# Kernel optimization log

Hardware: AMD Instinct MI355X
Metric: run time of the kernel (lower is better)

## Reference

```python
import jax, jax.numpy as jnp
import numpy as np

GROUP = 4      # number of groups in the batch dim
SHARED_GP = 4  # conv groups for q/k 1x1 convs
C = 512
N = 4096
B = 4          # B_all = GROUP * B = 16
EPS_LN = 1e-6
EPS_Z = 1e-6


def _phi(x):
    return jax.nn.relu(x) + 1.0


def _grouped_1x1(x, W):
    # x: [B, C, N], W: [g, C/g, C/g] block-diagonal 1x1 conv weights
    Bx, Cx, Nx = x.shape
    g = W.shape[0]
    xg = x.reshape(Bx, g, Cx // g, Nx)
    return jnp.einsum('goc,bgcn->bgon', W, xg).reshape(Bx, Cx, Nx)


def _ln(x, w, b, eps=EPS_LN):
    m = jnp.mean(x, axis=-1, keepdims=True)
    v = jnp.mean(jnp.square(x - m), axis=-1, keepdims=True)
    return (x - m) * jax.lax.rsqrt(v + eps) * w + b


def setup_inputs() -> dict:
    key = jax.random.key(0)
    ks = jax.random.split(key, 12)
    cg = C // SHARED_GP
    s = 1.0 / np.sqrt(C)
    return {
        'x': jax.random.normal(ks[0], (GROUP * B, C, N), dtype=jnp.float32),
        'Wq': jax.random.normal(ks[1], (SHARED_GP, cg, cg), dtype=jnp.float32) / np.sqrt(cg),
        'Wk': jax.random.normal(ks[2], (SHARED_GP, cg, cg), dtype=jnp.float32) / np.sqrt(cg),
        'Wv': jax.random.normal(ks[3], (C, C), dtype=jnp.float32) * s,
        'Wphi': jax.random.normal(ks[4], (C, C), dtype=jnp.float32) * s,
        'ln1_w': jnp.ones((C,), dtype=jnp.float32),
        'ln1_b': jnp.zeros((C,), dtype=jnp.float32),
        'fc1_w': jax.random.normal(ks[5], (4 * C, C), dtype=jnp.float32) * s,
        'fc1_b': jnp.zeros((4 * C,), dtype=jnp.float32),
        'fc2_w': jax.random.normal(ks[6], (C, 4 * C), dtype=jnp.float32) / np.sqrt(4 * C),
        'fc2_b': jnp.zeros((C,), dtype=jnp.float32),
        'ln2_w': jnp.ones((C,), dtype=jnp.float32),
        'ln2_b': jnp.zeros((C,), dtype=jnp.float32),
    }


def reference(x, Wq, Wk, Wv, Wphi, ln1_w, ln1_b, fc1_w, fc1_b, fc2_w, fc2_b, ln2_w, ln2_b):
    B_all, Cc, Nn = x.shape
    g = GROUP
    Bb = B_all // g
    first, rest = x[:Bb], x[Bb:]             # [B,C,N], [M,C,N] with M=(g-1)*B
    M = (g - 1) * Bb

    q = _phi(_grouped_1x1(rest, Wq))          # [M,C,N]
    k0 = _phi(_grouped_1x1(first, Wk))        # [B,C,N]
    v0 = jnp.einsum('oc,bcn->bon', Wv, first)  # [B,C,N]
    phi_first = jnp.einsum('oc,bcn->bon', Wphi, first)
    phi_rest = jnp.einsum('oc,bcn->bon', Wphi, rest)

    # expand first-group k/v across the (g-1) query groups
    k = jnp.broadcast_to(k0[None], (g - 1, Bb, Cc, Nn)).reshape(M, Cc, Nn)
    v = jnp.broadcast_to(v0[None], (g - 1, Bb, Cc, Nn)).reshape(M, Cc, Nn)

    Qg = jnp.broadcast_to(k0.mean(axis=2, keepdims=True)[None],
                          (g - 1, Bb, Cc, 1)).reshape(M, Cc, 1)
    alpha = jax.nn.softmax(jnp.sum(Qg * k, axis=1, keepdims=True), axis=-1) * Nn  # [M,1,N]
    k_hat = k * alpha

    # linear attention: kv = k_hat @ v^T / sqrt(C)
    kv = jnp.einsum('mcn,mdn->mcd', k_hat, v) / jnp.sqrt(jnp.asarray(Cc, x.dtype))  # [M,C,C]
    k_sum = jnp.sum(k_hat, axis=-1)                                  # [M,C]
    z = 1.0 / (jnp.einsum('mcn,mc->mn', q, k_sum)[:, None, :] + EPS_Z)  # [M,1,N]
    y = jnp.einsum('mcn,mcd->mdn', q, kv) * z * phi_rest              # [M,C,N]

    y_first = jnp.mean(y, axis=0, keepdims=True) * phi_first          # [B,C,N]
    out_first = _ln((first + y_first).transpose(0, 2, 1), ln1_w, ln1_b)  # [B,N,C]
    h = jax.nn.relu(out_first @ fc1_w.T + fc1_b)
    out_first = out_first + h @ fc2_w.T + fc2_b
    out_first = jax.nn.relu(_ln(out_first, ln2_w, ln2_b))
    out_first = out_first.transpose(0, 2, 1)                          # [B,C,N]
    return jnp.concatenate([out_first, rest], axis=0)
```

## Files before the change

kernel.cpp:

```cpp
#include <hip/hip_runtime.h>

#define N_DIM 4096
#define C_DIM 512
#define CN_ ((long)C_DIM * (long)N_DIM)

typedef unsigned short ushort_t;
typedef __attribute__((ext_vector_type(8))) short bf16x8;
typedef __attribute__((ext_vector_type(4))) float f32x4;

typedef const __attribute__((address_space(1))) unsigned int* gas_t;
typedef __attribute__((address_space(3))) unsigned int* las_t;
#define GLOAD(g, l) __builtin_amdgcn_global_load_lds((gas_t)(g), (las_t)(l), 16, 0, 0)

__device__ __forceinline__ ushort_t f2b(float f) {
    unsigned u = __builtin_bit_cast(unsigned, f);
    u += 0x7fffu + ((u >> 16) & 1u);
    return (ushort_t)(u >> 16);
}
__device__ __forceinline__ float b2f(ushort_t s) {
    return __builtin_bit_cast(float, (unsigned)s << 16);
}

enum { EPI_NONE = 0, EPI_PHI = 1, EPI_RELU_BIAS = 2, EPI_RES_BIAS = 3, EPI_PRE = 4 };

#define STAGE(q, koff) { \
    GLOAD(ap0 + (koff), &Als[q][la0]); \
    GLOAD(ap1 + (koff), &Als[q][la1]); \
    GLOAD(bp0 + (koff), &Bls[q][la0]); \
    GLOAD(bp1 + (koff), &Bls[q][la1]); }

#define COMPUTE(q) { \
    bf16x8 af[4], bfv[4]; \
    _Pragma("unroll") for (int m_ = 0; m_ < 4; ++m_) \
        af[m_] = *(const bf16x8*)&Als[q][(wr + m_ * 16 + fr) * 32 + rsw]; \
    _Pragma("unroll") for (int nf_ = 0; nf_ < 4; ++nf_) \
        bfv[nf_] = *(const bf16x8*)&Bls[q][(wc + nf_ * 16 + fr) * 32 + rsw]; \
    _Pragma("unroll") for (int m_ = 0; m_ < 4; ++m_) \
        _Pragma("unroll") for (int nf_ = 0; nf_ < 4; ++nf_) \
            acc[m_][nf_] = __builtin_amdgcn_mfma_f32_16x16x32_bf16( \
                af[m_], bfv[nf_], acc[m_][nf_], 0, 0, 0); }

#define KLOOP(K_) { \
    STAGE(0, 0); \
    __syncthreads(); \
    int kk_ = 0; \
    while (true) { \
        if (kk_ + 32 < (K_)) STAGE(1, kk_ + 32); \
        COMPUTE(0); \
        __syncthreads(); \
        kk_ += 32; \
        if (kk_ >= (K_)) break; \
        if (kk_ + 32 < (K_)) STAGE(0, kk_ + 32); \
        COMPUTE(1); \
        __syncthreads(); \
        kk_ += 32; \
        if (kk_ >= (K_)) break; \
    } }

template<int EPI, bool GROUPED, bool OBF, bool DEN, bool QGS>
__global__ __launch_bounds__(256, 3) void mfma_gemm(
    const ushort_t* __restrict__ Wb, const ushort_t* __restrict__ A,
    void* __restrict__ OUTV, const float* __restrict__ bias,
    const ushort_t* __restrict__ auxb, const float* __restrict__ auxf,
    int K, int O, int a_rstride, long a_zstride, long o_zstride, long auxb_zstride,
    int xt, int yt)
{
    __shared__ ushort_t Als[2][128 * 32];
    __shared__ ushort_t Bls[2][128 * 32];
    const int tid = threadIdx.x;

    const int L = blockIdx.x;
    const int gpx = (gridDim.x >> 3) / xt;
    const int xcd = L & 7;
    const int j = L >> 3;
    const int xtile = j % xt;
    const int g = xcd * gpx + j / xt;
    const int ytile = g % yt;
    const int z = g / yt;

    const int o0 = xtile * 128;
    const int n0 = ytile * 128;
    const ushort_t* Az = A + (long)z * a_zstride;
    const ushort_t* Wp = Wb;
    int kbase = 0, obase = o0;
    if (GROUPED) { int gg = o0 >> 7; Wp = Wb + (long)gg * (128 * 128); kbase = gg << 7; obase = 0; }

    const int w = tid >> 6, l = tid & 63;
    const int lr = l >> 2, lg = l & 3;
    const int rA0 = w * 32 + lr, rA1 = w * 32 + 16 + lr;
    const int gA0 = lg ^ ((rA0 >> 1) & 3), gA1 = lg ^ ((rA1 >> 1) & 3);
    const ushort_t* ap0 = Az + (long)(n0 + rA0) * a_rstride + kbase + gA0 * 8;
    const ushort_t* ap1 = Az + (long)(n0 + rA1) * a_rstride + kbase + gA1 * 8;
    const ushort_t* bp0 = Wp + (long)(obase + rA0) * K + gA0 * 8;
    const ushort_t* bp1 = Wp + (long)(obase + rA1) * K + gA1 * 8;
    const int la0 = (w * 32) * 32, la1 = (w * 32 + 16) * 32;

    const int wr = (w >> 1) * 64, wc = (w & 1) * 64;
    const int fr = l & 15, ks = l >> 4;
    const int rsw = (ks ^ ((fr >> 1) & 3)) << 3;

    f32x4 acc[4][4];
#pragma unroll
    for (int m = 0; m < 4; ++m)
#pragma unroll
        for (int nf = 0; nf < 4; ++nf) acc[m][nf] = f32x4{0.f, 0.f, 0.f, 0.f};

    KLOOP(K);

    float dsum[4][4];
    if (DEN) {
#pragma unroll
        for (int m = 0; m < 4; ++m)
#pragma unroll
            for (int j2 = 0; j2 < 4; ++j2) dsum[m][j2] = 0.f;
    }
    float qsum[4];
    if (QGS) {
#pragma unroll
        for (int nf = 0; nf < 4; ++nf) qsum[nf] = 0.f;
    }

#pragma unroll
    for (int m = 0; m < 4; ++m) {
#pragma unroll
        for (int nf = 0; nf < 4; ++nf) {
            const int oo = o0 + wc + nf * 16 + fr;
            float bval = 0.f;
            if (EPI == EPI_RELU_BIAS || EPI == EPI_RES_BIAS) bval = bias[oo];
            float kw = 0.f;
            if (DEN) kw = bias[((z & 3) << 9) + oo];
#pragma unroll
            for (int j2 = 0; j2 < 4; ++j2) {
                const int nn = n0 + wr + m * 16 + ks * 4 + j2;
                const long ridx = (long)nn * O + oo;
                float v = acc[m][nf][j2];
                if (EPI == EPI_PHI)            v = fmaxf(v, 0.f) + 1.f;
                else if (EPI == EPI_RELU_BIAS) v = fmaxf(v + bval, 0.f);
                else if (EPI == EPI_RES_BIAS)  v = v + bval + b2f(auxb[(long)z * auxb_zstride + ridx]);
                else if (EPI == EPI_PRE)       v = b2f(auxb[(long)z * auxb_zstride + ridx]) + auxf[ridx] * v;
                if (DEN) dsum[m][j2] += v * kw;
                if (QGS) qsum[nf] += v;
                if (OBF) ((ushort_t*)OUTV)[(long)z * o_zstride + ridx] = f2b(v);
                else     ((float*)OUTV)[(long)z * o_zstride + ridx] = v;
            }
        }
    }

    if (DEN) {
#pragma unroll
        for (int m = 0; m < 4; ++m)
#pragma unroll
            for (int j2 = 0; j2 < 4; ++j2) {
                float d = dsum[m][j2];
                d += __shfl_xor(d, 1); d += __shfl_xor(d, 2);
                d += __shfl_xor(d, 4); d += __shfl_xor(d, 8);
                if (fr == 0) {
                    const int nn = n0 + wr + m * 16 + ks * 4 + j2;
                    atomicAdd((float*)&auxf[(long)z * N_DIM + nn], d);
                }
            }
    }
    if (QGS) {
#pragma unroll
        for (int nf = 0; nf < 4; ++nf) {
            float d = qsum[nf];
            d += __shfl_xor(d, 16);
            d += __shfl_xor(d, 32);
            if (ks == 0) {
                const int oo = o0 + wc + nf * 16 + fr;
                atomicAdd((float*)&auxf[((long)z << 9) + oo], d);
            }
        }
    }
}

__global__ __launch_bounds__(256, 3) void kv_mfma(
    const ushort_t* __restrict__ v0c, const ushort_t* __restrict__ khat,
    float* __restrict__ kvp)
{
    __shared__ ushort_t Als[2][128 * 32];
    __shared__ ushort_t Bls[2][128 * 32];
    const int tid = threadIdx.x;
    const int L = blockIdx.x;
    const int gpx = (gridDim.x >> 3) >> 2;
    const int xcd = L & 7;
    const int j = L >> 3;
    const int xtile = j & 3;
    const int g = xcd * gpx + (j >> 2);
    const int ytile = g & 3;
    const int z = g >> 2;
    const int c0 = xtile * 128, d0 = ytile * 128;
    const int b = z >> 3, nch = z & 7;

    const int w = tid >> 6, l = tid & 63;
    const int lr = l >> 2, lg = l & 3;
    const int rA0 = w * 32 + lr, rA1 = w * 32 + 16 + lr;
    const int gA0 = lg ^ ((rA0 >> 1) & 3), gA1 = lg ^ ((rA1 >> 1) & 3);
    const ushort_t* Ab = v0c + (long)b * CN_ + nch * 512;
    const ushort_t* Bb = khat + (long)b * CN_ + nch * 512;
    const ushort_t* ap0 = Ab + (long)(d0 + rA0) * N_DIM + gA0 * 8;
    const ushort_t* ap1 = Ab + (long)(d0 + rA1) * N_DIM + gA1 * 8;
    const ushort_t* bp0 = Bb + (long)(c0 + rA0) * N_DIM + gA0 * 8;
    const ushort_t* bp1 = Bb + (long)(c0 + rA1) * N_DIM + gA1 * 8;
    const int la0 = (w * 32) * 32, la1 = (w * 32 + 16) * 32;

    const int wr = (w >> 1) * 64, wc = (w & 1) * 64;
    const int fr = l & 15, ks = l >> 4;
    const int rsw = (ks ^ ((fr >> 1) & 3)) << 3;

    f32x4 acc[4][4];
#pragma unroll
    for (int m = 0; m < 4; ++m)
#pragma unroll
        for (int nf = 0; nf < 4; ++nf) acc[m][nf] = f32x4{0.f, 0.f, 0.f, 0.f};

    KLOOP(512);

    float* KV = kvp + ((long)(nch * 4 + b)) * 262144;
#pragma unroll
    for (int m = 0; m < 4; ++m)
#pragma unroll
        for (int nf = 0; nf < 4; ++nf) {
            const int cc = c0 + wc + nf * 16 + fr;
#pragma unroll
            for (int j2 = 0; j2 < 4; ++j2) {
                const int dd = d0 + wr + m * 16 + ks * 4 + j2;
                KV[(long)dd * 512 + cc] = acc[m][nf][j2];
            }
        }
}

__global__ __launch_bounds__(256) void cvt_scale8(
    const float* __restrict__ kvp, ushort_t* __restrict__ out)
{
    const float s = 0.044194173824159216f;
    const long i = ((long)blockIdx.x * 256 + threadIdx.x) * 4;
    const int b = (int)(i >> 18);
    const long j = i & 262143;
    float4 a = make_float4(0.f, 0.f, 0.f, 0.f);
#pragma unroll
    for (int nch = 0; nch < 8; ++nch) {
        float4 v = *(const float4*)&kvp[((long)(nch * 4 + b)) * 262144 + j];
        a.x += v.x; a.y += v.y; a.z += v.z; a.w += v.w;
    }
    union { ushort_t sh[4]; uint2 u; } p;
    p.sh[0] = f2b(a.x * s); p.sh[1] = f2b(a.y * s);
    p.sh[2] = f2b(a.z * s); p.sh[3] = f2b(a.w * s);
    *(uint2*)&out[i] = p.u;
}

__global__ __launch_bounds__(256, 2) void ybar_gemm(
    const ushort_t* __restrict__ q12, const ushort_t* __restrict__ kvT,
    const ushort_t* __restrict__ xT12, const ushort_t* __restrict__ Wphi_b,
    const float* __restrict__ den12, ushort_t* __restrict__ y12)
{
    __shared__ ushort_t Als[2][128 * 32];
    __shared__ ushort_t Bls[2][128 * 32];
    __shared__ ushort_t Cls[2][128 * 32];
    __shared__ ushort_t Dls[2][128 * 32];
    const int tid = threadIdx.x;
    const int L = blockIdx.x;
    const int gpx = (gridDim.x >> 3) >> 2;
    const int xcd = L & 7;
    const int j = L >> 3;
    const int xtile = j & 3;
    const int g = xcd * gpx + (j >> 2);
    const int ytile = g & 31;
    const int mm = g >> 5;
    const int o0 = xtile * 128, n0 = ytile * 128;

    const int w = tid >> 6, l = tid & 63;
    const int lr = l >> 2, lg = l & 3;
    const int rA0 = w * 32 + lr, rA1 = w * 32 + 16 + lr;
    const int gA0 = lg ^ ((rA0 >> 1) & 3), gA1 = lg ^ ((rA1 >> 1) & 3);
    const long aoff0 = (long)(n0 + rA0) * 512 + gA0 * 8;
    const long aoff1 = (long)(n0 + rA1) * 512 + gA1 * 8;
    const long boff0 = (long)(o0 + rA0) * 512 + gA0 * 8;
    const long boff1 = (long)(o0 + rA1) * 512 + gA1 * 8;
    const int la0 = (w * 32) * 32, la1 = (w * 32 + 16) * 32;

    const int wr = (w >> 1) * 64, wc = (w & 1) * 64;
    const int fr = l & 15, ks = l >> 4;
    const int rsw = (ks ^ ((fr >> 1) & 3)) << 3;

    const ushort_t* pa0 = xT12 + (long)mm * CN_ + aoff0;
    const ushort_t* pa1 = xT12 + (long)mm * CN_ + aoff1;
    const ushort_t* pb0 = Wphi_b + boff0;
    const ushort_t* pb1 = Wphi_b + boff1;
    const ushort_t* qa0 = q12 + (long)mm * CN_ + aoff0;
    const ushort_t* qa1 = q12 + (long)mm * CN_ + aoff1;
    const ushort_t* kb0 = kvT + (long)(mm & 3) * 262144 + boff0;
    const ushort_t* kb1 = kvT + (long)(mm & 3) * 262144 + boff1;

    f32x4 accP[4][4], accQ[4][4];
#pragma unroll
    for (int m = 0; m < 4; ++m)
#pragma unroll
        for (int nf = 0; nf < 4; ++nf) {
            accP[m][nf] = f32x4{0.f, 0.f, 0.f, 0.f};
            accQ[m][nf] = f32x4{0.f, 0.f, 0.f, 0.f};
        }

#define STAGE2(q, koff) { \
    GLOAD(pa0 + (koff), &Als[q][la0]); GLOAD(pa1 + (koff), &Als[q][la1]); \
    GLOAD(pb0 + (koff), &Bls[q][la0]); GLOAD(pb1 + (koff), &Bls[q][la1]); \
    GLOAD(qa0 + (koff), &Cls[q][la0]); GLOAD(qa1 + (koff), &Cls[q][la1]); \
    GLOAD(kb0 + (koff), &Dls[q][la0]); GLOAD(kb1 + (koff), &Dls[q][la1]); }

#define COMPUTE2(q) { \
    bf16x8 af[4], bfv[4], cf[4], df[4]; \
    _Pragma("unroll") for (int m_ = 0; m_ < 4; ++m_) { \
        af[m_] = *(const bf16x8*)&Als[q][(wr + m_ * 16 + fr) * 32 + rsw]; \
        cf[m_] = *(const bf16x8*)&Cls[q][(wr + m_ * 16 + fr) * 32 + rsw]; } \
    _Pragma("unroll") for (int nf_ = 0; nf_ < 4; ++nf_) { \
        bfv[nf_] = *(const bf16x8*)&Bls[q][(wc + nf_ * 16 + fr) * 32 + rsw]; \
        df[nf_] = *(const bf16x8*)&Dls[q][(wc + nf_ * 16 + fr) * 32 + rsw]; } \
    _Pragma("unroll") for (int m_ = 0; m_ < 4; ++m_) \
        _Pragma("unroll") for (int nf_ = 0; nf_ < 4; ++nf_) { \
            accP[m_][nf_] = __builtin_amdgcn_mfma_f32_16x16x32_bf16( \
                af[m_], bfv[nf_], accP[m_][nf_], 0, 0, 0); \
            accQ[m_][nf_] = __builtin_amdgcn_mfma_f32_16x16x32_bf16( \
                cf[m_], df[nf_], accQ[m_][nf_], 0, 0, 0); } }

    STAGE2(0, 0);
    __syncthreads();
    int kk = 0;
    while (true) {
        if (kk + 32 < 512) STAGE2(1, kk + 32);
        COMPUTE2(0);
        __syncthreads();
        kk += 32;
        if (kk >= 512) break;
        if (kk + 32 < 512) STAGE2(0, kk + 32);
        COMPUTE2(1);
        __syncthreads();
        kk += 32;
        if (kk >= 512) break;
    }
#undef STAGE2
#undef COMPUTE2

    const float* D = den12 + (long)mm * N_DIM;
    ushort_t* Y = y12 + (long)mm * CN_;
#pragma unroll
    for (int m = 0; m < 4; ++m) {
        float zr[4];
#pragma unroll
        for (int j2 = 0; j2 < 4; ++j2)
            zr[j2] = 1.f / (D[n0 + wr + m * 16 + ks * 4 + j2] + 1e-6f);
#pragma unroll
        for (int nf = 0; nf < 4; ++nf) {
            const int oo = o0 + wc + nf * 16 + fr;
#pragma unroll
            for (int j2 = 0; j2 < 4; ++j2) {
                const int nn = n0 + wr + m * 16 + ks * 4 + j2;
                Y[(long)nn * 512 + oo] = f2b(accQ[m][nf][j2] * zr[j2] * accP[m][nf][j2]);
            }
        }
    }
}

__global__ __launch_bounds__(256) void ybar_reduce(
    const ushort_t* __restrict__ y12, float* __restrict__ ybar)
{
    const long i = ((long)blockIdx.x * 256 + threadIdx.x) * 8;
    float s[8] = {0.f, 0.f, 0.f, 0.f, 0.f, 0.f, 0.f, 0.f};
    for (int mm = 0; mm < 12; ++mm) {
        uint4 u = *(const uint4*)&y12[(long)mm * CN_ + i];
        const ushort_t* us = (const ushort_t*)&u;
#pragma unroll
        for (int j = 0; j < 8; ++j) s[j] += b2f(us[j]);
    }
#pragma unroll
    for (int j = 0; j < 8; ++j) s[j] *= (1.f / 12.f);
    *(float4*)&ybar[i] = make_float4(s[0], s[1], s[2], s[3]);
    *(float4*)&ybar[i + 4] = make_float4(s[4], s[5], s[6], s[7]);
}

template<int ALPHA>
__global__ __launch_bounds__(256) void transpose_b2b(
    const ushort_t* __restrict__ in, ushort_t* __restrict__ out,
    const float* __restrict__ alpha, float* __restrict__ ksum)
{
    __shared__ ushort_t t[64][72];
    const int tid = threadIdx.x;
    const int n0 = blockIdx.x * 64, c0 = blockIdx.y * 64, z = blockIdx.z;
    const ushort_t* I = in + (long)z * CN_;
    ushort_t* O = out + (long)z * CN_;
    const int r = tid >> 2, s8 = (tid & 3) * 16;
    uint4 u0 = *(const uint4*)&I[(long)(n0 + r) * 512 + c0 + s8];
    uint4 u1 = *(const uint4*)&I[(long)(n0 + r) * 512 + c0 + s8 + 8];
    *(uint4*)&t[r][s8] = u0;
    *(uint4*)&t[r][s8 + 8] = u1;
    __syncthreads();
    union { ushort_t sh[16]; uint4 u[2]; } p;
#pragma unroll
    for (int i = 0; i < 16; ++i) {
        ushort_t v = t[s8 + i][r];
        if (ALPHA) v = f2b(b2f(v) * alpha[(long)z * N_DIM + n0 + s8 + i]);
        p.sh[i] = v;
    }
    uint4* dst = (uint4*)&O[(long)(c0 + r) * N_DIM + n0 + s8];
    dst[0] = p.u[0]; dst[1] = p.u[1];
    if (ALPHA) {
        const int c = tid & 63, q = tid >> 6;
        float s = 0.f;
#pragma unroll
        for (int i = 0; i < 16; ++i) {
            const int n = q * 16 + i;
            s += b2f(t[n][c]) * alpha[(long)z * N_DIM + n0 + n];
        }
        atomicAdd(&ksum[((long)z << 9) + c0 + c], s);
    }
}

__global__ __launch_bounds__(256) void cvt_all(
    const float* __restrict__ s0, ushort_t* __restrict__ d0,
    const float* __restrict__ s1, ushort_t* __restrict__ d1,
    const float* __restrict__ s2, ushort_t* __restrict__ d2,
    const float* __restrict__ s3, ushort_t* __restrict__ d3,
    const float* __restrict__ s4, ushort_t* __restrict__ d4,
    const float* __restrict__ s5, ushort_t* __restrict__ d5)
{
    long i = ((long)blockIdx.x * 256 + threadIdx.x) * 4;
    const float* s; ushort_t* d; long off;
    if (i < 65536)        { s = s0; d = d0; off = i; }
    else if (i < 131072)  { s = s1; d = d1; off = i - 65536; }
    else if (i < 393216)  { s = s2; d = d2; off = i - 131072; }
    else if (i < 655360)  { s = s3; d = d3; off = i - 393216; }
    else if (i < 1703936) { s = s4; d = d4; off = i - 655360; }
    else                  { s = s5; d = d5; off = i - 1703936; }
    float4 v = *(const float4*)&s[off];
    union { ushort_t sh[4]; uint2 u; } p;
    p.sh[0] = f2b(v.x); p.sh[1] = f2b(v.y); p.sh[2] = f2b(v.z); p.sh[3] = f2b(v.w);
    *(uint2*)&d[off] = p.u;
}

template<int PASSZ>
__global__ __launch_bounds__(256) void transpose_f2b(
    const float* __restrict__ in, ushort_t* __restrict__ out,
    int rows, int cols, long in_z, long out_z, float* __restrict__ passout)
{
    __shared__ float t[64][65];
    const int tid = threadIdx.x;
    const int n0 = blockIdx.x * 64, c0 = blockIdx.y * 64;
    const int z = blockIdx.z;
    const float* I = in + (long)z * in_z;
    ushort_t* Ot = out + (long)z * out_z;
    const int r = tid >> 2, s4 = (tid & 3) * 16;
    float4 raw[4];
#pragma unroll
    for (int i = 0; i < 16; i += 4) {
        float4 v = *(const float4*)&I[(long)(c0 + r) * cols + n0 + s4 + i];
        raw[i >> 2] = v;
        t[r][s4 + i] = v.x; t[r][s4 + i + 1] = v.y;
        t[r][s4 + i + 2] = v.z; t[r][s4 + i + 3] = v.w;
    }
    if (PASSZ && z >= 4) {
        float* P = passout + (long)z * in_z + (long)(c0 + r) * cols + n0 + s4;
#pragma unroll
        for (int i = 0; i < 4; ++i) *(float4*)&P[i * 4] = raw[i];
    }
    __syncthreads();
    union { ushort_t s[16]; uint4 u[2]; } pk;
#pragma unroll
    for (int i = 0; i < 16; ++i) pk.s[i] = f2b(t[s4 + i][r]);
    uint4* dst = (uint4*)&Ot[(long)(n0 + r) * rows + c0 + s4];
    dst[0] = pk.u[0]; dst[1] = pk.u[1];
}

__global__ __launch_bounds__(256) void dot_rows(
    const ushort_t* __restrict__ X, const float* __restrict__ w,
    float* __restrict__ out, float scale)
{
    const int tid = threadIdx.x;
    const int rn = tid >> 2, cs = (tid & 3) * 128;
    const int z = blockIdx.y;
    const int n = blockIdx.x * 64 + rn;
    const ushort_t* row = X + (long)z * CN_ + (long)n * C_DIM;
    const float* wz = w + (long)(z & 3) * C_DIM;
    float s = 0.f;
    for (int i = 0; i < 128; i += 8) {
        uint4 u = *(const uint4*)&row[cs + i];
        const ushort_t* us = (const ushort_t*)&u;
#pragma unroll
        for (int k2 = 0; k2 < 8; ++k2) s += b2f(us[k2]) * wz[cs + i + k2];
    }
    s += __shfl_xor(s, 1); s += __shfl_xor(s, 2);
    if ((tid & 3) == 0) out[(long)z * N_DIM + n] = s * scale;
}

__global__ __launch_bounds__(256) void softmax_alpha(
    const float* __restrict__ logits, float* __restrict__ alpha)
{
    int b = blockIdx.x, tid = threadIdx.x;
    const float* L = logits + (long)b * N_DIM;
    float* A = alpha + (long)b * N_DIM;
    float lv[16];
    float mx = -3.4e38f;
#pragma unroll
    for (int i = 0; i < 4; i++) {
        float4 v = *(const float4*)&L[tid * 4 + i * 1024];
        lv[4 * i + 0] = v.x; lv[4 * i + 1] = v.y; lv[4 * i + 2] = v.z; lv[4 * i + 3] = v.w;
        mx = fmaxf(mx, fmaxf(fmaxf(v.x, v.y), fmaxf(v.z, v.w)));
    }
    __shared__ float red[8];
    float m = mx;
#pragma unroll
    for (int off = 32; off; off >>= 1) m = fmaxf(m, __shfl_down(m, off, 64));
    int wid = tid >> 6, lane = tid & 63;
    if (lane == 0) red[wid] = m;
    __syncthreads();
    m = fmaxf(fmaxf(red[0], red[1]), fmaxf(red[2], red[3]));
    float e[16], s = 0.f;
#pragma unroll
    for (int i = 0; i < 16; i++) { e[i] = expf(lv[i] - m); s += e[i]; }
#pragma unroll
    for (int off = 32; off; off >>= 1) s += __shfl_down(s, off, 64);
    if (lane == 0) red[4 + wid] = s;
    __syncthreads();
    float S = red[4] + red[5] + red[6] + red[7];
    float sc = 4096.f / S;
#pragma unroll
    for (int i = 0; i < 4; i++)
        *(float4*)&A[tid * 4 + i * 1024] =
            make_float4(e[4 * i] * sc, e[4 * i + 1] * sc, e[4 * i + 2] * sc, e[4 * i + 3] * sc);
}

template<int RELU, int OBF, int IBF>
__global__ __launch_bounds__(256) void ln_row(
    const void* __restrict__ inv, const float* __restrict__ g,
    const float* __restrict__ bt, void* __restrict__ outv)
{
    const int tid = threadIdx.x;
    const int r = tid >> 3, cs = (tid & 7) * 64;
    const long base = (((long)blockIdx.y * N_DIM) + blockIdx.x * 32 + r) * C_DIM + cs;
    float vv[64];
    float s = 0.f, s2 = 0.f;
    if (IBF) {
        const ushort_t* I = (const ushort_t*)inv + base;
#pragma unroll
        for (int i = 0; i < 8; ++i) {
            uint4 u = *(const uint4*)&I[i * 8];
            const ushort_t* us = (const ushort_t*)&u;
#pragma unroll
            for (int jj = 0; jj < 8; ++jj) {
                float f = b2f(us[jj]); vv[i * 8 + jj] = f; s += f; s2 += f * f;
            }
        }
    } else {
        const float* I = (const float*)inv + base;
#pragma unroll
        for (int i = 0; i < 16; ++i) {
            float4 v = *(const float4*)&I[i * 4];
            vv[i * 4] = v.x; vv[i * 4 + 1] = v.y; vv[i * 4 + 2] = v.z; vv[i * 4 + 3] = v.w;
            s += v.x + v.y + v.z + v.w;
            s2 += v.x * v.x + v.y * v.y + v.z * v.z + v.w * v.w;
        }
    }
#pragma unroll
    for (int off = 1; off < 8; off <<= 1) { s += __shfl_xor(s, off); s2 += __shfl_xor(s2, off); }
    const float mean = s * (1.f / 512.f);
    const float var = s2 * (1.f / 512.f) - mean * mean;
    const float rs = rsqrtf(var + 1e-6f);
#pragma unroll
    for (int i = 0; i < 64; i += 4) {
        float o[4];
#pragma unroll
        for (int jj = 0; jj < 4; ++jj) {
            float ov = (vv[i + jj] - mean) * rs * g[cs + i + jj] + bt[cs + i + jj];
            if (RELU) ov = fmaxf(ov, 0.f);
            o[jj] = ov;
        }
        if (OBF) {
            union { ushort_t s4[4]; uint2 u; } p;
            p.s4[0] = f2b(o[0]); p.s4[1] = f2b(o[1]); p.s4[2] = f2b(o[2]); p.s4[3] = f2b(o[3]);
            *(uint2*)&((ushort_t*)outv)[base + i] = p.u;
        } else {
            *(float4*)&((float*)outv)[base + i] = make_float4(o[0], o[1], o[2], o[3]);
        }
    }
}

__global__ __launch_bounds__(256) void ln_tr(
    const ushort_t* __restrict__ in, const float* __restrict__ g,
    const float* __restrict__ bt, float* __restrict__ out)
{
    __shared__ float t[32][513];
    const int tid = threadIdx.x;
    const int r = tid >> 3;
    const int lc = (tid & 7) * 8;
    const int z = blockIdx.y;
    const long n = (long)blockIdx.x * 32 + r;
    const ushort_t* I = in + ((long)z * N_DIM + n) * C_DIM;
    float vv[64];
    float s = 0.f, s2 = 0.f;
#pragma unroll
    for (int i = 0; i < 8; ++i) {
        const int c = i * 64 + lc;
        uint4 u = *(const uint4*)&I[c];
        const ushort_t* us = (const ushort_t*)&u;
#pragma unroll
        for (int jj = 0; jj < 8; ++jj) {
            float f = b2f(us[jj]); vv[i * 8 + jj] = f; s += f; s2 += f * f;
        }
    }
#pragma unroll
    for (int off = 1; off < 8; off <<= 1) { s += __shfl_xor(s, off); s2 += __shfl_xor(s2, off); }
    const float mean = s * (1.f / 512.f);
    const float var = s2 * (1.f / 512.f) - mean * mean;
    const float rs = rsqrtf(var + 1e-6f);
#pragma unroll
    for (int i = 0; i < 8; ++i) {
        const int c = i * 64 + lc;
#pragma unroll
        for (int jj = 0; jj < 8; ++jj) {
            float o = (vv[i * 8 + jj] - mean) * rs * g[c + jj] + bt[c + jj];
            t[r][c + jj] = fmaxf(o, 0.f);
        }
    }
    __syncthreads();
    float* O = out + (long)z * CN_ + (long)blockIdx.x * 32;
    for (int c = tid; c < 512; c += 256) {
        float* dst = O + (long)c * N_DIM;
#pragma unroll
        for (int i = 0; i < 32; i += 4)
            *(float4*)&dst[i] = make_float4(t[i][c], t[i + 1][c], t[i + 2][c], t[i + 3][c]);
    }
}

extern "C" void kernel_launch(void* const* d_in, const int* in_sizes, int n_in,
                              void* d_out, int out_size, void* d_ws, size_t ws_size,
                              hipStream_t stream)
{
    const float* x     = (const float*)d_in[0];
    const float* Wq    = (const float*)d_in[1];
    const float* Wk    = (const float*)d_in[2];
    const float* Wv    = (const float*)d_in[3];
    const float* Wphi  = (const float*)d_in[4];
    const float* ln1_w = (const float*)d_in[5];
    const float* ln1_b = (const float*)d_in[6];
    const float* fc1_w = (const float*)d_in[7];
    const float* fc1_bias = (const float*)d_in[8];
    const float* fc2_w = (const float*)d_in[9];
    const float* fc2_bias = (const float*)d_in[10];
    const float* ln2_w = (const float*)d_in[11];
    const float* ln2_b = (const float*)d_in[12];
    float* out = (float*)d_out;

    float* ws = (float*)d_ws;
    const long CN = CN_;
    ushort_t* xTfirst = (ushort_t*)ws;
    ushort_t* tln     = (ushort_t*)ws;
    ushort_t* xT12 = (ushort_t*)(ws + 2 * CN);
    ushort_t* hbuf4 = (ushort_t*)(ws + 2 * CN);
    ushort_t* q12   = (ushort_t*)(ws + 8 * CN);
    ushort_t* y12   = (ushort_t*)(ws + 14 * CN);
    ushort_t* k0b = (ushort_t*)(ws + 20 * CN);
    ushort_t* v0b = (ushort_t*)(ws + 22 * CN);
    ushort_t* pre_b = (ushort_t*)(ws + 20 * CN);
    ushort_t* khat = (ushort_t*)(ws + 24 * CN);
    ushort_t* v0c  = (ushort_t*)(ws + 26 * CN);
    ushort_t* ubuf_b = (ushort_t*)(ws + 24 * CN);
    float* ybar = ws + 32 * CN;
    float* kvp  = ws + 33 * CN;
    ushort_t* kvT = (ushort_t*)(ws + 33 * CN + 8388608);
    float* wb = ws + 33 * CN + 8388608 + 524288;
    ushort_t* Wk_b   = (ushort_t*)(wb);
    ushort_t* Wq_b   = (ushort_t*)(wb + 32768);
    ushort_t* Wv_b   = (ushort_t*)(wb + 65536);
    ushort_t* Wphi_b = (ushort_t*)(wb + 196608);
    ushort_t* fc1_b16 = (ushort_t*)(wb + 327680);
    ushort_t* fc2_b16 = (ushort_t*)(wb + 851968);
    float* Qg     = wb + 1376256;
    float* ksum   = wb + 1378304;
    float* logits = wb + 1380352;
    float* alpha  = wb + 1396736;
    float* den12  = wb + 1413120;

    dim3 blk(256);

    cvt_all<<<2688, blk, 0, stream>>>(Wk, Wk_b, Wq, Wq_b, Wv, Wv_b,
                                      Wphi, Wphi_b, fc1_w, fc1_b16, fc2_w, fc2_b16);
    hipMemsetAsync(Qg, 0, 4096 * sizeof(float), stream);
    hipMemsetAsync(den12, 0, 49152 * sizeof(float), stream);

    transpose_f2b<1><<<dim3(64, 8, 16), blk, 0, stream>>>(
        x, xTfirst, 512, 4096, CN, CN, out);

    mfma_gemm<EPI_PHI, true, true, false, true><<<512, blk, 0, stream>>>(
        Wk_b, xTfirst, k0b, nullptr, nullptr, Qg, 128, 512, 512, CN, CN, 0, 4, 32);
    mfma_gemm<EPI_NONE, false, true, false, false><<<512, blk, 0, stream>>>(
        Wv_b, xTfirst, v0b, nullptr, nullptr, nullptr, 512, 512, 512, CN, CN, 0, 4, 32);
    dot_rows<<<dim3(64, 4), blk, 0, stream>>>(k0b, Qg, logits, 1.f / 4096.f);
    softmax_alpha<<<4, blk, 0, stream>>>(logits, alpha);
    transpose_b2b<1><<<dim3(64, 8, 4), blk, 0, stream>>>(k0b, khat, alpha, ksum);
    transpose_b2b<0><<<dim3(64, 8, 4), blk, 0, stream>>>(v0b, v0c, nullptr, nullptr);
    kv_mfma<<<512, blk, 0, stream>>>(v0c, khat, kvp);
    cvt_scale8<<<1024, blk, 0, stream>>>(kvp, kvT);

    mfma_gemm<EPI_PHI, true, true, true, false><<<1536, blk, 0, stream>>>(
        Wq_b, xT12, q12, ksum, nullptr, den12, 128, 512, 512, CN, CN, 0, 4, 32);
    ybar_gemm<<<1536, blk, 0, stream>>>(q12, kvT, xT12, Wphi_b, den12, y12);
    ybar_reduce<<<1024, blk, 0, stream>>>(y12, ybar);

    mfma_gemm<EPI_PRE, false, true, false, false><<<512, blk, 0, stream>>>(
        Wphi_b, xTfirst, pre_b, nullptr, xTfirst, ybar, 512, 512, 512, CN, CN, CN, 4, 32);
    ln_row<0, 1, 1><<<dim3(128, 4), blk, 0, stream>>>(pre_b, ln1_w, ln1_b, tln);
    mfma_gemm<EPI_RELU_BIAS, false, true, false, false><<<2048, blk, 0, stream>>>(
        fc1_b16, tln, hbuf4, fc1_bias, nullptr, nullptr,
        512, 2048, 512, CN, 8388608, 0, 16, 32);
    mfma_gemm<EPI_RES_BIAS, false, true, false, false><<<512, blk, 0, stream>>>(
        fc2_b16, hbuf4, ubuf_b, fc2_bias, tln, nullptr,
        2048, 512, 2048, 8388608, CN, CN, 4, 32);
    ln_tr<<<dim3(128, 4), blk, 0, stream>>>(ubuf_b, ln2_w, ln2_b, out);
}
```

Baseline: 459.1 us.

## Prefetch two stages ahead with partial vmcnt waits in GEMM k-loops

Restructures the double-buffered k-loops so that two stages are in flight at once. Each iteration waits with an explicit s_waitcnt vmcnt that allows the newer stage's loads to stay outstanding, instead of waiting for everything at __syncthreads. Raw s_barrier calls wrapped in sched_barrier replace __syncthreads, so global-to-LDS loads can overlap MFMA compute across more than one step. Correctness now depends on the hand-counted vmcnt values matching the number of loads per stage (4 or 8), and the scheduling barriers limit compiler reordering.

Measured after the change: 452.7 us, median of 2. About the same (-1.4%).

```diff
diff --git a/kernel.cpp b/kernel.cpp
--- a/kernel.cpp
+++ b/kernel.cpp
@@ -22,6 +22,11 @@
 }
 
 enum { EPI_NONE = 0, EPI_PHI = 1, EPI_RELU_BIAS = 2, EPI_RES_BIAS = 3, EPI_PRE = 4 };
+
+#define SBAR { __builtin_amdgcn_sched_barrier(0); __builtin_amdgcn_s_barrier(); __builtin_amdgcn_sched_barrier(0); }
+#define WAITV0 { asm volatile("s_waitcnt vmcnt(0)" ::: "memory"); __builtin_amdgcn_sched_barrier(0); }
+#define WAITV4 { asm volatile("s_waitcnt vmcnt(4)" ::: "memory"); __builtin_amdgcn_sched_barrier(0); }
+#define WAITV8 { asm volatile("s_waitcnt vmcnt(8)" ::: "memory"); __builtin_amdgcn_sched_barrier(0); }
 
 #define STAGE(q, koff) { \
     GLOAD(ap0 + (koff), &Als[q][la0]); \
@@ -41,20 +46,18 @@
                 af[m_], bfv[nf_], acc[m_][nf_], 0, 0, 0); }
 
 #define KLOOP(K_) { \
+    const int S_ = (K_) / 32; \
     STAGE(0, 0); \
-    __syncthreads(); \
-    int kk_ = 0; \
+    if (S_ > 1) STAGE(1, 32); \
+    int s_ = 0; \
     while (true) { \
-        if (kk_ + 32 < (K_)) STAGE(1, kk_ + 32); \
-        COMPUTE(0); \
-        __syncthreads(); \
-        kk_ += 32; \
-        if (kk_ >= (K_)) break; \
-        if (kk_ + 32 < (K_)) STAGE(0, kk_ + 32); \
-        COMPUTE(1); \
-        __syncthreads(); \
-        kk_ += 32; \
-        if (kk_ >= (K_)) break; \
+        if (s_ + 1 < S_) { WAITV4 } else { WAITV0 } \
+        SBAR; \
+        COMPUTE(s_ & 1); \
+        SBAR; \
+        if (s_ + 2 < S_) STAGE(s_ & 1, (s_ + 2) * 32); \
+        ++s_; \
+        if (s_ >= S_) break; \
     } }
 
 template<int EPI, bool GROUPED, bool OBF, bool DEN, bool QGS>
@@ -323,19 +326,16 @@
                 cf[m_], df[nf_], accQ[m_][nf_], 0, 0, 0); } }
 
     STAGE2(0, 0);
-    __syncthreads();
-    int kk = 0;
+    STAGE2(1, 32);
+    int s_ = 0;
     while (true) {
-        if (kk + 32 < 512) STAGE2(1, kk + 32);
-        COMPUTE2(0);
-        __syncthreads();
-        kk += 32;
-        if (kk >= 512) break;
-        if (kk + 32 < 512) STAGE2(0, kk + 32);
-        COMPUTE2(1);
-        __syncthreads();
-        kk += 32;
-        if (kk >= 512) break;
+        if (s_ + 1 < 16) { WAITV8 } else { WAITV0 }
+        SBAR;
+        COMPUTE2(s_ & 1);
+        SBAR;
+        if (s_ + 2 < 16) STAGE2(s_ & 1, (s_ + 2) * 32);
+        ++s_;
+        if (s_ >= 16) break;
     }
 #undef STAGE2
 #undef COMPUTE2
```
